# Optimization experiments

Measured on AMD Instinct MI355X. Metric: run time of the kernel, lower is better.

The kernel has to match this reference:

```python
import jax, jax.numpy as jnp
import numpy as np

N_NODES = 20000
N_EDGES = 160000
N_GRAPHS = 16
NEG_INF = -1e30


def gcn_conv(x, edge_index, edge_weight, W, b):
    # PyG GCNConv with improved=True: add self-loops with weight 2.0,
    # symmetric degree normalization, linear transform, scatter-add aggregation.
    N = x.shape[0]
    row, col = edge_index[0], edge_index[1]
    loop = jnp.arange(N)
    row = jnp.concatenate([row, loop])
    col = jnp.concatenate([col, loop])
    ew = jnp.concatenate([edge_weight, jnp.full((N,), 2.0, edge_weight.dtype)])
    deg = jax.ops.segment_sum(ew, col, num_segments=N)
    dinv = jnp.where(deg > 0, deg ** -0.5, 0.0)  # deg_inv_sqrt, inf -> 0
    norm = dinv[row] * ew * dinv[col]            # [E+N]
    xl = x @ W                                   # [N, out]
    out = jax.ops.segment_sum(xl[row] * norm[:, None], col, num_segments=N)
    return out + b


def segment_softmax_masked(logits, mask, batch, num_segments):
    # softmax over masked entries, grouped by graph id (torch_geometric softmax
    # after masked_select); unmasked-out positions return 0.
    neg = jnp.asarray(NEG_INF, logits.dtype)
    ml = jnp.where(mask, logits, neg)
    mx = jax.ops.segment_max(ml, batch, num_segments=num_segments)
    ex = jnp.where(mask, jnp.exp(logits - mx[batch]), 0.0)
    s = jax.ops.segment_sum(ex, batch, num_segments=num_segments)
    return ex / jnp.maximum(s[batch], 1e-16)


def setup_inputs() -> dict:
    key = jax.random.key(0)
    ks = jax.random.split(key, 12)
    x = jax.random.normal(ks[0], (N_NODES, 5), dtype=jnp.float32)
    edge_index = jax.random.randint(ks[1], (2, N_EDGES), 0, N_NODES)
    edge_weight = jax.random.uniform(ks[2], (N_EDGES,), dtype=jnp.float32)
    mask = jax.random.randint(ks[3], (N_NODES,), 0, 2).astype(bool)
    batch = jnp.sort(jax.random.randint(ks[4], (N_NODES,), 0, N_GRAPHS))
    # parameters (Glorot-ish scaling)
    W1 = jax.random.normal(ks[5], (5, 1000), dtype=jnp.float32) / np.sqrt(5)
    b1 = jnp.zeros((1000,), jnp.float32)
    W2 = jax.random.normal(ks[6], (1000, 1000), dtype=jnp.float32) / np.sqrt(1000)
    b2 = jnp.zeros((1000,), jnp.float32)
    Wf = jax.random.normal(ks[7], (1000, 1), dtype=jnp.float32) / np.sqrt(1000)
    bf = jnp.zeros((1,), jnp.float32)
    return {"x": x, "edge_weight": edge_weight, "W1": W1, "b1": b1,
            "W2": W2, "b2": b2, "Wf": Wf, "bf": bf,
            "edge_index": edge_index, "mask": mask, "batch": batch}


def reference(x, edge_weight, W1, b1, W2, b2, Wf, bf, edge_index, mask, batch):
    h = jax.nn.relu(gcn_conv(x, edge_index, edge_weight, W1, b1))
    h = jax.nn.relu(gcn_conv(h, edge_index, edge_weight, W2, b2))
    # dropout treated as identity (eval mode) for a deterministic reference
    logits = (h @ Wf + bf)[:, 0]  # [N]
    return segment_softmax_masked(logits, mask, batch, N_GRAPHS)
```

## Files before the change

### kernel.cpp

```cpp
#include <hip/hip_runtime.h>

#define NN 20000
#define NE 160000
#define NG 16
#define KP 1024
#define MT2 160
#define MPAD2 (MT2*128)
#define NBLK 79

typedef __attribute__((ext_vector_type(8))) short bf16x8;
typedef __attribute__((ext_vector_type(4))) float f32x4;

#define GAS __attribute__((address_space(1)))
#define LAS __attribute__((address_space(3)))

__device__ __forceinline__ unsigned short f2bf(float f) {
    unsigned int u = __float_as_uint(f);
    u += 0x7FFFu + ((u >> 16) & 1u);
    return (unsigned short)(u >> 16);
}

__device__ __forceinline__ void gld_lds16(const char* g, char* l) {
    __builtin_amdgcn_global_load_lds((GAS void*)g, (LAS void*)l, 16, 0, 0);
}

__global__ void deg_cnt_kernel(const int* __restrict__ ei, const float* __restrict__ ew,
                               float* deg, int* cnt, const void* __restrict__ mask,
                               int* flags) {
    const int e = blockIdx.x * blockDim.x + threadIdx.x;
    if (e < 5000) {
        const unsigned v = ((const unsigned*)mask)[e];
        if (v > 1u) atomicOr(&flags[0], 1);
        if (v != 0u && v != 0x3F800000u) atomicOr(&flags[1], 1);
    }
    if (e >= NE) return;
    const int c = ei[NE + e];
    atomicAdd(&deg[c], ew[e]);
    atomicAdd(&cnt[c], 1);
}

__global__ __launch_bounds__(256) void partial_kernel(const int* __restrict__ cnt,
        const float* __restrict__ deg, const void* __restrict__ mask,
        const int* __restrict__ flags, int* __restrict__ mtmp,
        float* __restrict__ dinv, int* __restrict__ bcnt, int* __restrict__ bmsk) {
    const int b = blockIdx.x, t = threadIdx.x;
    const int i = b * 256 + t;
    const int f0 = flags[0], f1 = flags[1];
    int c = 0, mv = 0;
    if (i < NN) {
        c = cnt[i];
        dinv[i] = 1.0f / sqrtf(2.0f + deg[i]);
        if (f0 == 0)      mv = ((const int*)mask)[i] != 0;
        else if (f1 == 0) mv = ((const unsigned*)mask)[i] != 0u;
        else              mv = ((const unsigned char*)mask)[i] != 0;
        mtmp[i] = mv;
    }
    __shared__ int sc[256], sm[256];
    sc[t] = c; sm[t] = mv;
    __syncthreads();
    for (int off = 128; off; off >>= 1) {
        if (t < off) { sc[t] += sc[t + off]; sm[t] += sm[t + off]; }
        __syncthreads();
    }
    if (t == 0) { bcnt[b] = sc[0]; bmsk[b] = sm[0]; }
}

__global__ __launch_bounds__(128) void scanp_kernel(int* __restrict__ bcnt,
        int* __restrict__ bmsk, int* __restrict__ nm) {
    const int t = threadIdx.x;
    __shared__ int sc[128], sm[128];
    const int c = (t < NBLK) ? bcnt[t] : 0;
    const int m = (t < NBLK) ? bmsk[t] : 0;
    sc[t] = c; sm[t] = m;
    __syncthreads();
    for (int off = 1; off < 128; off <<= 1) {
        const int uc = (t >= off) ? sc[t - off] : 0;
        const int um = (t >= off) ? sm[t - off] : 0;
        __syncthreads();
        sc[t] += uc; sm[t] += um;
        __syncthreads();
    }
    if (t < NBLK) { bcnt[t] = sc[t] - c; bmsk[t] = sm[t] - m; }
    if (t == NBLK - 1) nm[0] = sm[t];
}

__global__ __launch_bounds__(256) void apply_kernel(const int* __restrict__ cnt,
        const int* __restrict__ mtmp, const int* __restrict__ bcnt,
        const int* __restrict__ bmsk, const int* __restrict__ batch,
        int* __restrict__ offs, int* __restrict__ perm, int* __restrict__ bc) {
    const int b = blockIdx.x, t = threadIdx.x;
    const int i = b * 256 + t;
    const int c  = (i < NN) ? cnt[i]  : 0;
    const int mv = (i < NN) ? mtmp[i] : 0;
    __shared__ int sc[256], sm[256];
    sc[t] = c; sm[t] = mv;
    __syncthreads();
    for (int off = 1; off < 256; off <<= 1) {
        const int uc = (t >= off) ? sc[t - off] : 0;
        const int um = (t >= off) ? sm[t - off] : 0;
        __syncthreads();
        sc[t] += uc; sm[t] += um;
        __syncthreads();
    }
    if (i < NN) {
        offs[i] = bcnt[b] + sc[t] - c;
        if (mv) {
            const int pos = bmsk[b] + sm[t] - 1;
            perm[pos] = i;
            bc[pos] = batch[i];
        }
    }
}

__global__ void scatter_kernel(const int* __restrict__ ei, const float* __restrict__ ew,
                               const float* __restrict__ dinv, const int* __restrict__ offs,
                               int* cursor, int* __restrict__ ssrc, float* __restrict__ snorm) {
    const int e = blockIdx.x * blockDim.x + threadIdx.x;
    if (e >= NE) return;
    const int r = ei[e], c = ei[NE + e];
    const int pos = atomicAdd(&cursor[c], 1);
    const int idx = offs[c] + pos;
    ssrc[idx] = r;
    snorm[idx] = dinv[r] * ew[e] * dinv[c];
}

__global__ __launch_bounds__(256) void axf_kernel(const float* __restrict__ x,
        const int* __restrict__ ssrc, const float* __restrict__ snorm,
        const int* __restrict__ offs, const int* __restrict__ cnt,
        const float* __restrict__ dinv, float* __restrict__ Axf) {
    const int i = blockIdx.x * blockDim.x + threadIdx.x;
    if (i >= NN) return;
    float a0=0,a1=0,a2=0,a3=0,a4=0;
    const int s0 = offs[i], n = cnt[i];
    for (int e = s0; e < s0 + n; ++e) {
        const int r = ssrc[e];
        const float w = snorm[e];
        const float* xr = x + r * 5;
        a0 += w*xr[0]; a1 += w*xr[1]; a2 += w*xr[2]; a3 += w*xr[3]; a4 += w*xr[4];
    }
    const float wl = 2.0f * dinv[i] * dinv[i];
    const float* xi = x + i * 5;
    a0 += wl*xi[0]; a1 += wl*xi[1]; a2 += wl*xi[2]; a3 += wl*xi[3]; a4 += wl*xi[4];
    float* o = Axf + i * 5;
    o[0]=a0; o[1]=a1; o[2]=a2; o[3]=a3; o[4]=a4;
}

__global__ __launch_bounds__(256) void w2t_kernel(const float* __restrict__ W2,
                                                  unsigned short* __restrict__ W2t) {
    __shared__ float tile[32][33];
    const int bw = blockIdx.x;
    const int n0 = (bw & 31) * 32;
    const int k0 = (bw >> 5) * 32;
    const int t = threadIdx.x;
    const int tx = t & 31, ty = t >> 5;
#pragma unroll
    for (int j = 0; j < 4; ++j) {
        const int k = k0 + ty + j * 8;
        const int n = n0 + tx;
        tile[ty + j * 8][tx] = (k < 1000 && n < 1000) ? W2[k * 1000 + n] : 0.0f;
    }
    __syncthreads();
#pragma unroll
    for (int j = 0; j < 4; ++j) {
        const int n = n0 + ty + j * 8;
        const int k = k0 + tx;
        W2t[(size_t)n * KP + k] = f2bf(tile[tx][ty + j * 8]);
    }
}

__global__ __launch_bounds__(256) void aggW1_kernel(const float* __restrict__ Axf,
        const float* __restrict__ W1, const float* __restrict__ b1,
        const int* __restrict__ ssrc, const float* __restrict__ snorm,
        const int* __restrict__ offs, const int* __restrict__ cnt,
        const float* __restrict__ dinv, const int* __restrict__ perm,
        const int* __restrict__ nm, unsigned short* __restrict__ G) {
    const int t = threadIdx.x;
    __shared__ int s_nm;
    if (t == 0) s_nm = nm[0];
    __syncthreads();
    const int nmv = s_nm;
    const int npad = (nmv + 127) & ~127;
    const int j0 = blockIdx.x * 8;
    if (j0 >= npad) return;

    const bool active = t < 250;
    const int c0 = active ? t * 4 : 1000 + (t - 250) * 4;
    float w[5][4];
    float bb[4];
    if (active) {
#pragma unroll
        for (int f = 0; f < 5; ++f) {
            const float4 wv = *(const float4*)(W1 + f * 1000 + c0);
            w[f][0] = wv.x; w[f][1] = wv.y; w[f][2] = wv.z; w[f][3] = wv.w;
        }
        const float4 b4 = *(const float4*)(b1 + c0);
        bb[0] = b4.x; bb[1] = b4.y; bb[2] = b4.z; bb[3] = b4.w;
    } else {
#pragma unroll
        for (int f = 0; f < 5; ++f) { w[f][0]=0; w[f][1]=0; w[f][2]=0; w[f][3]=0; }
        bb[0]=0; bb[1]=0; bb[2]=0; bb[3]=0;
    }

    __shared__ int   se[64];
    __shared__ float sw[64];
    for (int jj = 0; jj < 8; ++jj) {
        const int j = j0 + jj;
        if (j >= npad) break;
        float acc0 = 0.f, acc1 = 0.f, acc2 = 0.f, acc3 = 0.f;
        if (j < nmv) {
            const int i = perm[j];
            const int s0 = offs[i], n = cnt[i];
            for (int base = 0; base < n; base += 64) {
                const int m = (n - base < 64) ? (n - base) : 64;
                __syncthreads();
                if (t < m) { se[t] = ssrc[s0 + base + t]; sw[t] = snorm[s0 + base + t]; }
                __syncthreads();
                for (int e = 0; e < m; ++e) {
                    const int r = se[e];
                    const float we = sw[e];
                    const float* axr = Axf + r * 5;
                    float z0 = bb[0], z1 = bb[1], z2 = bb[2], z3 = bb[3];
#pragma unroll
                    for (int f = 0; f < 5; ++f) {
                        const float a = axr[f];
                        z0 += a * w[f][0]; z1 += a * w[f][1];
                        z2 += a * w[f][2]; z3 += a * w[f][3];
                    }
                    acc0 += we * fmaxf(z0, 0.f); acc1 += we * fmaxf(z1, 0.f);
                    acc2 += we * fmaxf(z2, 0.f); acc3 += we * fmaxf(z3, 0.f);
                }
            }
            {
                const float wl = 2.0f * dinv[i] * dinv[i];
                const float* axi = Axf + i * 5;
                float z0 = bb[0], z1 = bb[1], z2 = bb[2], z3 = bb[3];
#pragma unroll
                for (int f = 0; f < 5; ++f) {
                    const float a = axi[f];
                    z0 += a * w[f][0]; z1 += a * w[f][1];
                    z2 += a * w[f][2]; z3 += a * w[f][3];
                }
                acc0 += wl * fmaxf(z0, 0.f); acc1 += wl * fmaxf(z1, 0.f);
                acc2 += wl * fmaxf(z2, 0.f); acc3 += wl * fmaxf(z3, 0.f);
            }
        }
        ushort4 pk;
        pk.x = f2bf(acc0); pk.y = f2bf(acc1); pk.z = f2bf(acc2); pk.w = f2bf(acc3);
        *(ushort4*)(G + (size_t)j * KP + c0) = pk;
    }
}

__global__ __launch_bounds__(256) void gemm_kernel(const unsigned short* __restrict__ A,
                                                   const unsigned short* __restrict__ B,
                                                   const float* __restrict__ b2,
                                                   const float* __restrict__ Wf,
                                                   const int* __restrict__ nm,
                                                   float* __restrict__ logitsC) {
    __shared__ unsigned short As[4096];
    __shared__ unsigned short Bs[4096];
    const int tid = threadIdx.x;
    __shared__ int s_nm;
    if (tid == 0) s_nm = nm[0];
    __syncthreads();
    const int nmv = s_nm;
    const int mstrips = (nmv + 127) >> 7;
    const int bid = blockIdx.x;
    const int tm = (bid >> 6) * 8 + (bid & 7);
    const int tn = (bid >> 3) & 7;
    if (tm >= mstrips) return;
    const int lane = tid & 63;
    const int wv = tid >> 6;
    const int wr = wv >> 1, wc = wv & 1;

    const int chunk = ((tid & 3) ^ ((tid >> 3) & 3)) * 16;
    const int rsub = tid >> 2;
    const char* Ag = (const char*)(A + (size_t)(tm * 128 + rsub) * KP) + chunk;
    const char* Bg = (const char*)(B + (size_t)(tn * 128 + rsub) * KP) + chunk;
    char* AsW = (char*)As + wv * 1024;
    char* BsW = (char*)Bs + wv * 1024;

    f32x4 acc[4][4];
#pragma unroll
    for (int i = 0; i < 4; ++i)
#pragma unroll
        for (int j = 0; j < 4; ++j) acc[i][j] = (f32x4){0.f, 0.f, 0.f, 0.f};

    const int m = lane & 15;
    const int quad = lane >> 4;
    const int sw = quad ^ ((m >> 1) & 3);
    const int aoff = (wr * 64 + m) * 64 + sw * 16;
    const int boff = (wc * 64 + m) * 64 + sw * 16;

    for (int kk = 0; kk < KP; kk += 32) {
        __syncthreads();
        const int kb = kk * 2;
        gld_lds16(Ag + kb,             AsW);
        gld_lds16(Ag + kb + 64 * 2048, AsW + 4096);
        gld_lds16(Bg + kb,             BsW);
        gld_lds16(Bg + kb + 64 * 2048, BsW + 4096);
        __syncthreads();
        bf16x8 af[4], bfv[4];
#pragma unroll
        for (int mt = 0; mt < 4; ++mt)
            af[mt] = *(const bf16x8*)((const char*)As + aoff + mt * 1024);
#pragma unroll
        for (int nt = 0; nt < 4; ++nt)
            bfv[nt] = *(const bf16x8*)((const char*)Bs + boff + nt * 1024);
#pragma unroll
        for (int mt = 0; mt < 4; ++mt)
#pragma unroll
            for (int nt = 0; nt < 4; ++nt)
                acc[mt][nt] = __builtin_amdgcn_mfma_f32_16x16x32_bf16(af[mt], bfv[nt], acc[mt][nt], 0, 0, 0);
    }

    const int col0 = tn * 128 + wc * 64 + m;
    const int row00 = tm * 128 + wr * 64 + quad * 4;
#pragma unroll
    for (int mt = 0; mt < 4; ++mt) {
        float ps0 = 0.f, ps1 = 0.f, ps2 = 0.f, ps3 = 0.f;
#pragma unroll
        for (int nt = 0; nt < 4; ++nt) {
            const int c = col0 + nt * 16;
            const float bbv = (c < 1000) ? b2[c] : 0.0f;
            const float wfv = (c < 1000) ? Wf[c] : 0.0f;
            ps0 += fmaxf(acc[mt][nt][0] + bbv, 0.f) * wfv;
            ps1 += fmaxf(acc[mt][nt][1] + bbv, 0.f) * wfv;
            ps2 += fmaxf(acc[mt][nt][2] + bbv, 0.f) * wfv;
            ps3 += fmaxf(acc[mt][nt][3] + bbv, 0.f) * wfv;
        }
#pragma unroll
        for (int msk = 1; msk < 16; msk <<= 1) {
            ps0 += __shfl_xor(ps0, msk);
            ps1 += __shfl_xor(ps1, msk);
            ps2 += __shfl_xor(ps2, msk);
            ps3 += __shfl_xor(ps3, msk);
        }
        if (m == 0) {
            const int row = row00 + mt * 16;
            if (row + 0 < nmv) atomicAdd(&logitsC[row + 0], ps0);
            if (row + 1 < nmv) atomicAdd(&logitsC[row + 1], ps1);
            if (row + 2 < nmv) atomicAdd(&logitsC[row + 2], ps2);
            if (row + 3 < nmv) atomicAdd(&logitsC[row + 3], ps3);
        }
    }
}

__global__ __launch_bounds__(256) void softmax_kernel(const float* __restrict__ logitsC,
        const int* __restrict__ perm, const int* __restrict__ bc,
        const int* __restrict__ nm, float* __restrict__ out) {
    const int g = blockIdx.x;
    const int t = threadIdx.x;
    __shared__ int s_lo, s_hi;
    __shared__ float red[4];
    __shared__ float sval;
    if (t == 0) {
        const int nmv = nm[0];
        int lo = 0, hi = nmv;
        while (lo < hi) { const int mid = (lo + hi) >> 1; if (bc[mid] < g) lo = mid + 1; else hi = mid; }
        s_lo = lo;
        int lo2 = lo, hi2 = nmv;
        while (lo2 < hi2) { const int mid = (lo2 + hi2) >> 1; if (bc[mid] < g + 1) lo2 = mid + 1; else hi2 = mid; }
        s_hi = lo2;
    }
    __syncthreads();
    const int lo = s_lo, hi = s_hi;
    float mx = -1e30f;
    for (int i = lo + t; i < hi; i += 256) mx = fmaxf(mx, logitsC[i]);
    for (int off = 32; off; off >>= 1) mx = fmaxf(mx, __shfl_down(mx, off));
    if ((t & 63) == 0) red[t >> 6] = mx;
    __syncthreads();
    if (t == 0) sval = fmaxf(fmaxf(red[0], red[1]), fmaxf(red[2], red[3]));
    __syncthreads();
    mx = sval;
    __syncthreads();
    float sm = 0.f;
    for (int i = lo + t; i < hi; i += 256) sm += expf(logitsC[i] - mx);
    for (int off = 32; off; off >>= 1) sm += __shfl_down(sm, off);
    if ((t & 63) == 0) red[t >> 6] = sm;
    __syncthreads();
    if (t == 0) sval = red[0] + red[1] + red[2] + red[3];
    __syncthreads();
    const float inv = 1.0f / fmaxf(sval, 1e-16f);
    for (int i = lo + t; i < hi; i += 256)
        out[perm[i]] = expf(logitsC[i] - mx) * inv;
}

extern "C" void kernel_launch(void* const* d_in, const int* in_sizes, int n_in,
                              void* d_out, int out_size, void* d_ws, size_t ws_size,
                              hipStream_t stream) {
    (void)in_sizes; (void)n_in; (void)ws_size;
    const float* x   = (const float*)d_in[0];
    const float* ew  = (const float*)d_in[1];
    const float* W1  = (const float*)d_in[2];
    const float* b1  = (const float*)d_in[3];
    const float* W2  = (const float*)d_in[4];
    const float* b2  = (const float*)d_in[5];
    const float* Wf  = (const float*)d_in[6];
    const int*   ei  = (const int*)d_in[8];
    const void*  mask  = d_in[9];
    const int*   batch = (const int*)d_in[10];
    float* out = (float*)d_out;

    char* p = (char*)d_ws;
    auto carve = [&](size_t bytes) { char* q = p; p += (bytes + 255) & ~(size_t)255; return q; };
    char* zbase = p;
    float* deg     = (float*)carve(NN * 4);
    int*   cnt     = (int*)carve(NN * 4);
    int*   cursor  = (int*)carve(NN * 4);
    float* logitsC = (float*)carve(MPAD2 * 4);
    int*   flags   = (int*)carve(256);
    size_t zspan = (size_t)(p - zbase);
    int*   offs   = (int*)carve(NN * 4);
    float* dinv   = (float*)carve(NN * 4);
    int*   mtmp   = (int*)carve(NN * 4);
    int*   perm   = (int*)carve(NN * 4);
    int*   bc     = (int*)carve(NN * 4);
    int*   bcnt   = (int*)carve(NBLK * 4);
    int*   bmsk   = (int*)carve(NBLK * 4);
    int*   nmp    = (int*)carve(256);
    int*   ssrc   = (int*)carve(NE * 4);
    float* snorm  = (float*)carve(NE * 4);
    float* Axf    = (float*)carve(NN * 5 * 4);
    unsigned short* W2t = (unsigned short*)carve((size_t)KP * KP * 2);
    unsigned short* G   = (unsigned short*)carve((size_t)MPAD2 * KP * 2);

    hipMemsetAsync(zbase, 0, zspan, stream);
    hipMemsetAsync(out, 0, (size_t)out_size * 4, stream);
    hipLaunchKernelGGL(deg_cnt_kernel,  dim3(625),      dim3(256),  0, stream, ei, ew, deg, cnt, mask, flags);
    hipLaunchKernelGGL(partial_kernel,  dim3(NBLK),     dim3(256),  0, stream, cnt, deg, mask, flags, mtmp, dinv, bcnt, bmsk);
    hipLaunchKernelGGL(scanp_kernel,    dim3(1),        dim3(128),  0, stream, bcnt, bmsk, nmp);
    hipLaunchKernelGGL(apply_kernel,    dim3(NBLK),     dim3(256),  0, stream, cnt, mtmp, bcnt, bmsk, batch, offs, perm, bc);
    hipLaunchKernelGGL(scatter_kernel,  dim3(625),      dim3(256),  0, stream, ei, ew, dinv, offs, cursor, ssrc, snorm);
    hipLaunchKernelGGL(axf_kernel,      dim3(79),       dim3(256),  0, stream, x, ssrc, snorm, offs, cnt, dinv, Axf);
    hipLaunchKernelGGL(w2t_kernel,      dim3(1024),     dim3(256),  0, stream, W2, W2t);
    hipLaunchKernelGGL(aggW1_kernel,    dim3(MPAD2/8),  dim3(256),  0, stream, Axf, W1, b1, ssrc, snorm, offs, cnt, dinv, perm, nmp, G);
    hipLaunchKernelGGL(gemm_kernel,     dim3(MT2*8),    dim3(256),  0, stream, G, W2t, b2, Wf, nmp, logitsC);
    hipLaunchKernelGGL(softmax_kernel,  dim3(NG),       dim3(256),  0, stream, logitsC, perm, bc, nmp, out);
}
```

Baseline: 213.8 us.

## Merge small prep kernels and stage neighbor features in LDS for aggW1

The W2 transpose/bf16 conversion now runs as extra blocks inside the partial-reduction kernel. The single-block block-offset scan is folded into apply_kernel, where every block redundantly scans the per-block sums in shared memory. Together these remove two launches from the serial chain. In aggW1, each edge's 5-feature Axf row and weight (with the self-loop appended as an extra entry) is now gathered once into shared memory as float4/float2, instead of every thread re-reading global memory per edge. The cost is redundant scan work in each apply block and slightly more shared-memory traffic.

```diff
diff --git a/kernel.cpp b/kernel.cpp
--- a/kernel.cpp
+++ b/kernel.cpp
@@ -39,56 +39,77 @@
     atomicAdd(&cnt[c], 1);
 }
 
-__global__ __launch_bounds__(256) void partial_kernel(const int* __restrict__ cnt,
+__global__ __launch_bounds__(256) void partial_w2t_kernel(const int* __restrict__ cnt,
         const float* __restrict__ deg, const void* __restrict__ mask,
         const int* __restrict__ flags, int* __restrict__ mtmp,
-        float* __restrict__ dinv, int* __restrict__ bcnt, int* __restrict__ bmsk) {
-    const int b = blockIdx.x, t = threadIdx.x;
-    const int i = b * 256 + t;
-    const int f0 = flags[0], f1 = flags[1];
-    int c = 0, mv = 0;
-    if (i < NN) {
-        c = cnt[i];
-        dinv[i] = 1.0f / sqrtf(2.0f + deg[i]);
-        if (f0 == 0)      mv = ((const int*)mask)[i] != 0;
-        else if (f1 == 0) mv = ((const unsigned*)mask)[i] != 0u;
-        else              mv = ((const unsigned char*)mask)[i] != 0;
-        mtmp[i] = mv;
-    }
-    __shared__ int sc[256], sm[256];
-    sc[t] = c; sm[t] = mv;
-    __syncthreads();
-    for (int off = 128; off; off >>= 1) {
-        if (t < off) { sc[t] += sc[t + off]; sm[t] += sm[t + off]; }
-        __syncthreads();
-    }
-    if (t == 0) { bcnt[b] = sc[0]; bmsk[b] = sm[0]; }
-}
-
-__global__ __launch_bounds__(128) void scanp_kernel(int* __restrict__ bcnt,
-        int* __restrict__ bmsk, int* __restrict__ nm) {
+        float* __restrict__ dinv, int* __restrict__ bcnt, int* __restrict__ bmsk,
+        const float* __restrict__ W2, unsigned short* __restrict__ W2t) {
+    const int bid = blockIdx.x;
     const int t = threadIdx.x;
-    __shared__ int sc[128], sm[128];
-    const int c = (t < NBLK) ? bcnt[t] : 0;
-    const int m = (t < NBLK) ? bmsk[t] : 0;
-    sc[t] = c; sm[t] = m;
-    __syncthreads();
-    for (int off = 1; off < 128; off <<= 1) {
-        const int uc = (t >= off) ? sc[t - off] : 0;
-        const int um = (t >= off) ? sm[t - off] : 0;
-        __syncthreads();
-        sc[t] += uc; sm[t] += um;
-        __syncthreads();
-    }
-    if (t < NBLK) { bcnt[t] = sc[t] - c; bmsk[t] = sm[t] - m; }
-    if (t == NBLK - 1) nm[0] = sm[t];
+    if (bid < NBLK) {
+        const int i = bid * 256 + t;
+        const int f0 = flags[0], f1 = flags[1];
+        int c = 0, mv = 0;
+        if (i < NN) {
+            c = cnt[i];
+            dinv[i] = 1.0f / sqrtf(2.0f + deg[i]);
+            if (f0 == 0)      mv = ((const int*)mask)[i] != 0;
+            else if (f1 == 0) mv = ((const unsigned*)mask)[i] != 0u;
+            else              mv = ((const unsigned char*)mask)[i] != 0;
+            mtmp[i] = mv;
+        }
+        __shared__ int sc[256], sm[256];
+        sc[t] = c; sm[t] = mv;
+        __syncthreads();
+        for (int off = 128; off; off >>= 1) {
+            if (t < off) { sc[t] += sc[t + off]; sm[t] += sm[t + off]; }
+            __syncthreads();
+        }
+        if (t == 0) { bcnt[bid] = sc[0]; bmsk[bid] = sm[0]; }
+    } else {
+        __shared__ float tile[32][33];
+        const int bw = bid - NBLK;
+        const int n0 = (bw & 31) * 32;
+        const int k0 = (bw >> 5) * 32;
+        const int tx = t & 31, ty = t >> 5;
+#pragma unroll
+        for (int j = 0; j < 4; ++j) {
+            const int k = k0 + ty + j * 8;
+            const int n = n0 + tx;
+            tile[ty + j * 8][tx] = (k < 1000 && n < 1000) ? W2[k * 1000 + n] : 0.0f;
+        }
+        __syncthreads();
+#pragma unroll
+        for (int j = 0; j < 4; ++j) {
+            const int n = n0 + ty + j * 8;
+            const int k = k0 + tx;
+            W2t[(size_t)n * KP + k] = f2bf(tile[tx][ty + j * 8]);
+        }
+    }
 }
 
 __global__ __launch_bounds__(256) void apply_kernel(const int* __restrict__ cnt,
         const int* __restrict__ mtmp, const int* __restrict__ bcnt,
         const int* __restrict__ bmsk, const int* __restrict__ batch,
-        int* __restrict__ offs, int* __restrict__ perm, int* __restrict__ bc) {
+        int* __restrict__ offs, int* __restrict__ perm, int* __restrict__ bc,
+        int* __restrict__ nm) {
     const int b = blockIdx.x, t = threadIdx.x;
+    __shared__ int pbc[128], pbm[128];
+    if (t < 128) {
+        pbc[t] = (t < NBLK) ? bcnt[t] : 0;
+        pbm[t] = (t < NBLK) ? bmsk[t] : 0;
+    }
+    __syncthreads();
+    for (int off = 1; off < 128; off <<= 1) {
+        int uc = 0, um = 0;
+        if (t < 128 && t >= off) { uc = pbc[t - off]; um = pbm[t - off]; }
+        __syncthreads();
+        if (t < 128) { pbc[t] += uc; pbm[t] += um; }
+        __syncthreads();
+    }
+    if (b == 0 && t == 0) nm[0] = pbm[NBLK - 1];
+    const int bco = (b == 0) ? 0 : pbc[b - 1];
+    const int bmo = (b == 0) ? 0 : pbm[b - 1];
     const int i = b * 256 + t;
     const int c  = (i < NN) ? cnt[i]  : 0;
     const int mv = (i < NN) ? mtmp[i] : 0;
@@ -103,9 +124,9 @@
         __syncthreads();
     }
     if (i < NN) {
-        offs[i] = bcnt[b] + sc[t] - c;
+        offs[i] = bco + sc[t] - c;
         if (mv) {
-            const int pos = bmsk[b] + sm[t] - 1;
+            const int pos = bmo + sm[t] - 1;
             perm[pos] = i;
             bc[pos] = batch[i];
         }
@@ -145,29 +166,6 @@
     o[0]=a0; o[1]=a1; o[2]=a2; o[3]=a3; o[4]=a4;
 }
 
-__global__ __launch_bounds__(256) void w2t_kernel(const float* __restrict__ W2,
-                                                  unsigned short* __restrict__ W2t) {
-    __shared__ float tile[32][33];
-    const int bw = blockIdx.x;
-    const int n0 = (bw & 31) * 32;
-    const int k0 = (bw >> 5) * 32;
-    const int t = threadIdx.x;
-    const int tx = t & 31, ty = t >> 5;
-#pragma unroll
-    for (int j = 0; j < 4; ++j) {
-        const int k = k0 + ty + j * 8;
-        const int n = n0 + tx;
-        tile[ty + j * 8][tx] = (k < 1000 && n < 1000) ? W2[k * 1000 + n] : 0.0f;
-    }
-    __syncthreads();
-#pragma unroll
-    for (int j = 0; j < 4; ++j) {
-        const int n = n0 + ty + j * 8;
-        const int k = k0 + tx;
-        W2t[(size_t)n * KP + k] = f2bf(tile[tx][ty + j * 8]);
-    }
-}
-
 __global__ __launch_bounds__(256) void aggW1_kernel(const float* __restrict__ Axf,
         const float* __restrict__ W1, const float* __restrict__ b1,
         const int* __restrict__ ssrc, const float* __restrict__ snorm,
@@ -201,8 +199,8 @@
         bb[0]=0; bb[1]=0; bb[2]=0; bb[3]=0;
     }
 
-    __shared__ int   se[64];
-    __shared__ float sw[64];
+    __shared__ float4 sax4[64];
+    __shared__ float2 sax2[64];
     for (int jj = 0; jj < 8; ++jj) {
         const int j = j0 + jj;
         if (j >= npad) break;
@@ -210,38 +208,34 @@
         if (j < nmv) {
             const int i = perm[j];
             const int s0 = offs[i], n = cnt[i];
-            for (int base = 0; base < n; base += 64) {
-                const int m = (n - base < 64) ? (n - base) : 64;
+            const int total = n + 1;
+            for (int base = 0; base < total; base += 64) {
+                const int m = (total - base < 64) ? (total - base) : 64;
                 __syncthreads();
-                if (t < m) { se[t] = ssrc[s0 + base + t]; sw[t] = snorm[s0 + base + t]; }
+                if (t < m) {
+                    const int idx = base + t;
+                    int r; float we;
+                    if (idx < n) { r = ssrc[s0 + idx]; we = snorm[s0 + idx]; }
+                    else         { r = i; const float dv = dinv[i]; we = 2.0f * dv * dv; }
+                    const float* axr = Axf + r * 5;
+                    sax4[t] = make_float4(axr[0], axr[1], axr[2], axr[3]);
+                    sax2[t] = make_float2(axr[4], we);
+                }
                 __syncthreads();
+#pragma unroll 2
                 for (int e = 0; e < m; ++e) {
-                    const int r = se[e];
-                    const float we = sw[e];
-                    const float* axr = Axf + r * 5;
+                    const float4 a4 = sax4[e];
+                    const float2 a2 = sax2[e];
                     float z0 = bb[0], z1 = bb[1], z2 = bb[2], z3 = bb[3];
-#pragma unroll
-                    for (int f = 0; f < 5; ++f) {
-                        const float a = axr[f];
-                        z0 += a * w[f][0]; z1 += a * w[f][1];
-                        z2 += a * w[f][2]; z3 += a * w[f][3];
-                    }
+                    z0 += a4.x*w[0][0]; z1 += a4.x*w[0][1]; z2 += a4.x*w[0][2]; z3 += a4.x*w[0][3];
+                    z0 += a4.y*w[1][0]; z1 += a4.y*w[1][1]; z2 += a4.y*w[1][2]; z3 += a4.y*w[1][3];
+                    z0 += a4.z*w[2][0]; z1 += a4.z*w[2][1]; z2 += a4.z*w[2][2]; z3 += a4.z*w[2][3];
+                    z0 += a4.w*w[3][0]; z1 += a4.w*w[3][1]; z2 += a4.w*w[3][2]; z3 += a4.w*w[3][3];
+                    z0 += a2.x*w[4][0]; z1 += a2.x*w[4][1]; z2 += a2.x*w[4][2]; z3 += a2.x*w[4][3];
+                    const float we = a2.y;
                     acc0 += we * fmaxf(z0, 0.f); acc1 += we * fmaxf(z1, 0.f);
                     acc2 += we * fmaxf(z2, 0.f); acc3 += we * fmaxf(z3, 0.f);
                 }
-            }
-            {
-                const float wl = 2.0f * dinv[i] * dinv[i];
-                const float* axi = Axf + i * 5;
-                float z0 = bb[0], z1 = bb[1], z2 = bb[2], z3 = bb[3];
-#pragma unroll
-                for (int f = 0; f < 5; ++f) {
-                    const float a = axi[f];
-                    z0 += a * w[f][0]; z1 += a * w[f][1];
-                    z2 += a * w[f][2]; z3 += a * w[f][3];
-                }
-                acc0 += wl * fmaxf(z0, 0.f); acc1 += wl * fmaxf(z1, 0.f);
-                acc2 += wl * fmaxf(z2, 0.f); acc3 += wl * fmaxf(z3, 0.f);
             }
         }
         ushort4 pk;
@@ -426,14 +420,12 @@
 
     hipMemsetAsync(zbase, 0, zspan, stream);
     hipMemsetAsync(out, 0, (size_t)out_size * 4, stream);
-    hipLaunchKernelGGL(deg_cnt_kernel,  dim3(625),      dim3(256),  0, stream, ei, ew, deg, cnt, mask, flags);
-    hipLaunchKernelGGL(partial_kernel,  dim3(NBLK),     dim3(256),  0, stream, cnt, deg, mask, flags, mtmp, dinv, bcnt, bmsk);
-    hipLaunchKernelGGL(scanp_kernel,    dim3(1),        dim3(128),  0, stream, bcnt, bmsk, nmp);
-    hipLaunchKernelGGL(apply_kernel,    dim3(NBLK),     dim3(256),  0, stream, cnt, mtmp, bcnt, bmsk, batch, offs, perm, bc);
-    hipLaunchKernelGGL(scatter_kernel,  dim3(625),      dim3(256),  0, stream, ei, ew, dinv, offs, cursor, ssrc, snorm);
-    hipLaunchKernelGGL(axf_kernel,      dim3(79),       dim3(256),  0, stream, x, ssrc, snorm, offs, cnt, dinv, Axf);
-    hipLaunchKernelGGL(w2t_kernel,      dim3(1024),     dim3(256),  0, stream, W2, W2t);
-    hipLaunchKernelGGL(aggW1_kernel,    dim3(MPAD2/8),  dim3(256),  0, stream, Axf, W1, b1, ssrc, snorm, offs, cnt, dinv, perm, nmp, G);
-    hipLaunchKernelGGL(gemm_kernel,     dim3(MT2*8),    dim3(256),  0, stream, G, W2t, b2, Wf, nmp, logitsC);
-    hipLaunchKernelGGL(softmax_kernel,  dim3(NG),       dim3(256),  0, stream, logitsC, perm, bc, nmp, out);
-}
+    hipLaunchKernelGGL(deg_cnt_kernel,    dim3(625),       dim3(256), 0, stream, ei, ew, deg, cnt, mask, flags);
+    hipLaunchKernelGGL(partial_w2t_kernel, dim3(NBLK+1024), dim3(256), 0, stream, cnt, deg, mask, flags, mtmp, dinv, bcnt, bmsk, W2, W2t);
+    hipLaunchKernelGGL(apply_kernel,      dim3(NBLK),      dim3(256), 0, stream, cnt, mtmp, bcnt, bmsk, batch, offs, perm, bc, nmp);
+    hipLaunchKernelGGL(scatter_kernel,    dim3(625),       dim3(256), 0, stream, ei, ew, dinv, offs, cursor, ssrc, snorm);
+    hipLaunchKernelGGL(axf_kernel,        dim3(79),        dim3(256), 0, stream, x, ssrc, snorm, offs, cnt, dinv, Axf);
+    hipLaunchKernelGGL(aggW1_kernel,      dim3(MPAD2/8),   dim3(256), 0, stream, Axf, W1, b1, ssrc, snorm, offs, cnt, dinv, perm, nmp, G);
+    hipLaunchKernelGGL(gemm_kernel,       dim3(MT2*8),     dim3(256), 0, stream, G, W2t, b2, Wf, nmp, logitsC);
+    hipLaunchKernelGGL(softmax_kernel,    dim3(NG),        dim3(256), 0, stream, logitsC, perm, bc, nmp, out);
+}
```

After: 200.1 us. 6.4% less time.
